# Kernel tuning notes

Hardware: AMD Instinct MI355X
Metric: run time of the kernel (lower is better)

## Reference

```python
import jax, jax.numpy as jnp
import numpy as np

D = 128
NM = 1043
ND = 2166
EM = 300000
ED = 600000


def _gcn(x, src, dst, w, W, b):
    # symmetric-normalized weighted GCN conv: out = A_norm @ (x W^T) + b
    n = x.shape[0]
    deg = jax.ops.segment_sum(w, dst, num_segments=n)
    dinv = jnp.where(deg > 0, 1.0 / jnp.sqrt(deg), 0.0)
    norm = dinv[src] * w * dinv[dst]          # [E]
    h = x @ W.T                               # [n, D]
    return jax.ops.segment_sum(h[src] * norm[:, None], dst, num_segments=n) + b


def _encoder(x, edge, w, W1, b1, W2, b2):
    src, dst = edge[0], edge[1]
    x1 = jax.nn.relu(_gcn(x, src, dst, w, W1, b1))
    x2 = jax.nn.relu(_gcn(x1, src, dst, w, W2, b2))
    return x1, x2


def _layer_view_att(x, fc1_W, fc1_b, fc2_W, fc2_b):
    # x: [C, D, N]; channel attention over views/layers (LayerViewAttention)
    a = x.mean(axis=(1, 2))                            # global avg pool -> [C]
    a = jax.nn.relu(a @ fc1_W.T + fc1_b)
    a = jax.nn.sigmoid(a @ fc2_W.T + fc2_b)
    return jax.nn.relu(x * a[:, None, None])


def _fcn(x, W1, b1, W2, b2):
    # Fcn fusion: Linear -> ReLU -> Linear -> ReLU
    h = jax.nn.relu(x @ W1.T + b1)
    return jax.nn.relu(h @ W2.T + b2)


def setup_inputs():
    key = jax.random.key(0)
    ks = iter(jax.random.split(key, 64))

    def nrm(shape, s=0.05):
        return jax.random.normal(next(ks), shape, jnp.float32) * s

    inp = {}
    inp["mirna_x"] = jax.random.normal(next(ks), (NM, D), jnp.float32)
    inp["drug_x"] = jax.random.normal(next(ks), (ND, D), jnp.float32)
    for pre, n, e in [("m1", NM, EM), ("m2", NM, EM), ("d1", ND, ED), ("d2", ND, ED)]:
        inp[pre + "_edge"] = jax.random.randint(next(ks), (2, e), 0, n, jnp.int32)
        inp[pre + "_w"] = jax.random.uniform(next(ks), (e,), jnp.float32)
        inp[pre + "_W1"] = nrm((D, D))
        inp[pre + "_b1"] = jnp.zeros((D,), jnp.float32)
        inp[pre + "_W2"] = nrm((D, D))
        inp[pre + "_b2"] = jnp.zeros((D,), jnp.float32)
    inp["m_fc1_W"] = nrm((4, 4)); inp["m_fc1_b"] = jnp.zeros((4,), jnp.float32)
    inp["m_fc2_W"] = nrm((4, 4)); inp["m_fc2_b"] = jnp.zeros((4,), jnp.float32)
    inp["d_fc1_W"] = nrm((2, 2)); inp["d_fc1_b"] = jnp.zeros((2,), jnp.float32)
    inp["d_fc2_W"] = nrm((2, 2)); inp["d_fc2_b"] = jnp.zeros((2,), jnp.float32)
    inp["m_fus_W1"] = nrm((2 * D, 4 * D)); inp["m_fus_b1"] = jnp.zeros((2 * D,), jnp.float32)
    inp["m_fus_W2"] = nrm((D, 2 * D));     inp["m_fus_b2"] = jnp.zeros((D,), jnp.float32)
    inp["d_fus_W1"] = nrm((2 * D, 2 * D)); inp["d_fus_b1"] = jnp.zeros((2 * D,), jnp.float32)
    inp["d_fus_W2"] = nrm((D, 2 * D));     inp["d_fus_b2"] = jnp.zeros((D,), jnp.float32)
    return inp


def reference(mirna_x, drug_x,
              m1_edge, m1_w, m1_W1, m1_b1, m1_W2, m1_b2,
              m2_edge, m2_w, m2_W1, m2_b1, m2_W2, m2_b2,
              d1_edge, d1_w, d1_W1, d1_b1, d1_W2, d1_b2,
              d2_edge, d2_w, d2_W1, d2_b1, d2_W2, d2_b2,
              m_fc1_W, m_fc1_b, m_fc2_W, m_fc2_b,
              d_fc1_W, d_fc1_b, d_fc2_W, d_fc2_b,
              m_fus_W1, m_fus_b1, m_fus_W2, m_fus_b2,
              d_fus_W1, d_fus_b1, d_fus_W2, d_fus_b2):
    # miRNA: 2 views x 2 layers -> 4 channels
    m1a, m1b = _encoder(mirna_x, m1_edge, m1_w, m1_W1, m1_b1, m1_W2, m1_b2)
    m2a, m2b = _encoder(mirna_x, m2_edge, m2_w, m2_W1, m2_b1, m2_W2, m2_b2)
    mx = jnp.stack([m1a, m1b, m2a, m2b], axis=0).transpose(0, 2, 1)   # [4, D, NM]
    mx = _layer_view_att(mx, m_fc1_W, m_fc1_b, m_fc2_W, m_fc2_b)
    m_out = _fcn(mx.transpose(2, 0, 1).reshape(NM, 4 * D),
                 m_fus_W1, m_fus_b1, m_fus_W2, m_fus_b2)             # [NM, D]
    # drug: views summed per layer -> 2 channels
    d1a, d1b = _encoder(drug_x, d1_edge, d1_w, d1_W1, d1_b1, d1_W2, d1_b2)
    d2a, d2b = _encoder(drug_x, d2_edge, d2_w, d2_W1, d2_b1, d2_W2, d2_b2)
    dx = jnp.stack([d1a + d2a, d1b + d2b], axis=0).transpose(0, 2, 1)  # [2, D, ND]
    dx = _layer_view_att(dx, d_fc1_W, d_fc1_b, d_fc2_W, d_fc2_b)
    d_out = _fcn(dx.transpose(2, 0, 1).reshape(ND, 2 * D),
                 d_fus_W1, d_fus_b1, d_fus_W2, d_fus_b2)             # [ND, D]
    return jnp.concatenate([m_out, d_out], axis=0)                   # [NM+ND, D]
```

## Files before the change

### kernel.cpp

```cpp
#include <hip/hip_runtime.h>
#include <math.h>

#define D128 128
#define NM_ 1043
#define ND_ 2166
#define EM_ 300000
#define ED_ 600000
#define NBH 64
#define NMAX 2176
#define NTOT 6418
#define ETOT 1800000

struct ViewArgs {
    const int* edge[4];
    const float* w[4];
    int n[4], E[4];
    int cumn[5];
    int cumE[5];
    int rpo[4];
};

struct BiasArr { const float* b[4]; };

__global__ __launch_bounds__(1024) void hist_b(ViewArgs va, int* __restrict__ pcnt,
                                               float* __restrict__ pdeg) {
    __shared__ int lc[NMAX];
    __shared__ float ld[NMAX];
    const int view = blockIdx.x >> 6, vb = blockIdx.x & 63;
    const int n = va.n[view], E = va.E[view];
    const int* edge = va.edge[view];
    const float* w = va.w[view];
    for (int i = threadIdx.x; i < n; i += 1024) { lc[i] = 0; ld[i] = 0.f; }
    __syncthreads();
    const int per = (E + NBH - 1) / NBH;
    const int b = vb * per, e = min(E, b + per);
    for (int i = b + threadIdx.x; i < e; i += 1024) {
        int dst = edge[E + i];
        atomicAdd(&lc[dst], 1);
        atomicAdd(&ld[dst], w[i]);
    }
    __syncthreads();
    int* pc = pcnt + (size_t)NBH * va.cumn[view] + (size_t)vb * n;
    float* pd = pdeg + (size_t)NBH * va.cumn[view] + (size_t)vb * n;
    for (int i = threadIdx.x; i < n; i += 1024) { pc[i] = lc[i]; pd[i] = ld[i]; }
}

__global__ void colred_b(ViewArgs va, const int* __restrict__ pcnt,
                         const float* __restrict__ pdeg, int* __restrict__ cnt,
                         float* __restrict__ dinv) {
    int i = blockIdx.x * 256 + threadIdx.x;
    if (i >= NTOT) return;
    int view = 0;
    while (view < 3 && i >= va.cumn[view + 1]) ++view;
    const int il = i - va.cumn[view], n = va.n[view];
    const int* pc = pcnt + (size_t)NBH * va.cumn[view];
    const float* pd = pdeg + (size_t)NBH * va.cumn[view];
    int c = 0;
    float dg = 0.f;
    for (int b = 0; b < NBH; ++b) {
        c += pc[(size_t)b * n + il];
        dg += pd[(size_t)b * n + il];
    }
    cnt[i] = c;
    dinv[i] = dg > 0.f ? 1.0f / sqrtf(dg) : 0.f;
}

__global__ void scan_b(ViewArgs va, const int* __restrict__ cnt, int* __restrict__ rowptr) {
    __shared__ int wsum[4];
    const int view = blockIdx.x;
    const int n = va.n[view];
    const int* c = cnt + va.cumn[view];
    int* rp = rowptr + va.rpo[view];
    const int tid = threadIdx.x;
    const int per = (n + 255) / 256;
    const int b0 = tid * per, e0 = min(n, b0 + per);
    int s = 0;
    for (int i = b0; i < e0; ++i) s += c[i];
    const int lane = tid & 63, wid = tid >> 6;
    int sc = s;
    for (int off = 1; off < 64; off <<= 1) {
        int t = __shfl_up(sc, off);
        if (lane >= off) sc += t;
    }
    if (lane == 63) wsum[wid] = sc;
    __syncthreads();
    int wbase = 0;
    for (int wv = 0; wv < wid; ++wv) wbase += wsum[wv];
    int run = wbase + sc - s;
    if (tid == 0) rp[0] = 0;
    for (int i = b0; i < e0; ++i) {
        run += c[i];
        rp[i + 1] = run;
    }
}

__global__ void cum_b(ViewArgs va, const int* __restrict__ pcnt,
                      const int* __restrict__ rowptr, int* __restrict__ cum) {
    int i = blockIdx.x * 256 + threadIdx.x;
    if (i >= NTOT) return;
    int view = 0;
    while (view < 3 && i >= va.cumn[view + 1]) ++view;
    const int il = i - va.cumn[view], n = va.n[view];
    const int* pc = pcnt + (size_t)NBH * va.cumn[view];
    int* cm = cum + (size_t)NBH * va.cumn[view];
    int run = rowptr[va.rpo[view] + il];
    for (int b = 0; b < NBH; ++b) {
        cm[(size_t)b * n + il] = run;
        run += pc[(size_t)b * n + il];
    }
}

__global__ __launch_bounds__(1024) void fill2_b(ViewArgs va, const float* __restrict__ dinv,
                                                const int* __restrict__ cum,
                                                int2* __restrict__ spair) {
    __shared__ int lc[NMAX];
    const int view = blockIdx.x >> 6, vb = blockIdx.x & 63;
    const int n = va.n[view], E = va.E[view];
    const int* edge = va.edge[view];
    const float* w = va.w[view];
    const int* cm = cum + (size_t)NBH * va.cumn[view] + (size_t)vb * n;
    const float* dv = dinv + va.cumn[view];
    int2* sp = spair + va.cumE[view];
    for (int i = threadIdx.x; i < n; i += 1024) lc[i] = cm[i];
    __syncthreads();
    const int per = (E + NBH - 1) / NBH;
    const int b = vb * per, e = min(E, b + per);
    for (int i = b + threadIdx.x; i < e; i += 1024) {
        int src = edge[i];
        int dst = edge[E + i];
        int pos = atomicAdd(&lc[dst], 1);
        float nrm = dv[src] * w[i] * dv[dst];
        sp[pos] = make_int2(src, __float_as_int(nrm));
    }
}

__global__ __launch_bounds__(128) void agg_b(ViewArgs va, const int2* __restrict__ spair,
                                             const int* __restrict__ rowptr,
                                             const float* __restrict__ h, BiasArr ba,
                                             float* __restrict__ outbuf) {
    const int xcd = blockIdx.x & 7, k = blockIdx.x >> 3;
    const int nf = (xcd < 2 ? xcd * 803 : 2 * 803 + (xcd - 2) * 802) + k;
    int view = 0;
    while (view < 3 && nf >= va.cumn[view + 1]) ++view;
    const int ln = nf - va.cumn[view];
    const int* rp = rowptr + va.rpo[view];
    const int beg = rp[ln], end = rp[ln + 1];
    const int2* sp = spair + va.cumE[view];
    const float* hb = h + (size_t)va.cumn[view] * D128;
    const int tid = threadIdx.x;
    float a0 = 0.f, a1 = 0.f, a2 = 0.f, a3 = 0.f;
    int i = beg;
    for (; i + 32 <= end; i += 32) {
        int4 q[16];
        float hv[32];
#pragma unroll
        for (int u = 0; u < 16; ++u) q[u] = *(const int4*)(sp + i + 2 * u);
#pragma unroll
        for (int u = 0; u < 16; ++u) {
            hv[2 * u] = hb[(size_t)q[u].x * D128 + tid];
            hv[2 * u + 1] = hb[(size_t)q[u].z * D128 + tid];
        }
#pragma unroll
        for (int u = 0; u < 16; ++u) {
            a0 = fmaf(__int_as_float(q[u].y), hv[2 * u], a0);
            a1 = fmaf(__int_as_float(q[u].w), hv[2 * u + 1], a1);
        }
    }
    for (; i + 8 <= end; i += 8) {
        int4 q0 = *(const int4*)(sp + i);
        int4 q1 = *(const int4*)(sp + i + 2);
        int4 q2 = *(const int4*)(sp + i + 4);
        int4 q3 = *(const int4*)(sp + i + 6);
        float h0 = hb[(size_t)q0.x * D128 + tid];
        float h1 = hb[(size_t)q0.z * D128 + tid];
        float h2 = hb[(size_t)q1.x * D128 + tid];
        float h3 = hb[(size_t)q1.z * D128 + tid];
        float h4 = hb[(size_t)q2.x * D128 + tid];
        float h5 = hb[(size_t)q2.z * D128 + tid];
        float h6 = hb[(size_t)q3.x * D128 + tid];
        float h7 = hb[(size_t)q3.z * D128 + tid];
        a0 = fmaf(__int_as_float(q0.y), h0, a0);
        a1 = fmaf(__int_as_float(q0.w), h1, a1);
        a2 = fmaf(__int_as_float(q1.y), h2, a2);
        a3 = fmaf(__int_as_float(q1.w), h3, a3);
        a0 = fmaf(__int_as_float(q2.y), h4, a0);
        a1 = fmaf(__int_as_float(q2.w), h5, a1);
        a2 = fmaf(__int_as_float(q3.y), h6, a2);
        a3 = fmaf(__int_as_float(q3.w), h7, a3);
    }
    for (; i + 4 <= end; i += 4) {
        int2 p0 = sp[i], p1 = sp[i + 1], p2 = sp[i + 2], p3 = sp[i + 3];
        a0 = fmaf(__int_as_float(p0.y), hb[(size_t)p0.x * D128 + tid], a0);
        a1 = fmaf(__int_as_float(p1.y), hb[(size_t)p1.x * D128 + tid], a1);
        a2 = fmaf(__int_as_float(p2.y), hb[(size_t)p2.x * D128 + tid], a2);
        a3 = fmaf(__int_as_float(p3.y), hb[(size_t)p3.x * D128 + tid], a3);
    }
    for (; i < end; ++i)
        a0 = fmaf(__int_as_float(sp[i].y), hb[(size_t)sp[i].x * D128 + tid], a0);
    float v = (a0 + a1) + (a2 + a3);
    outbuf[(size_t)nf * D128 + tid] = fmaxf(v + ba.b[view][tid], 0.f);
}

struct GSeg {
    const float* A;
    const float* W;
    const float* bias;
    float* C;
    int M, N, K, rowblks, blk0, relu;
};
struct GArgs { GSeg s[4]; int nseg; };

__global__ __launch_bounds__(256) void gemm_b(GArgs ga) {
    __shared__ float xs[32 * 64];
    __shared__ float wsm[128 * 64];
    int si = 0;
    while (si + 1 < ga.nseg && (int)blockIdx.x >= ga.s[si + 1].blk0) ++si;
    const GSeg S = ga.s[si];
    const int lb = blockIdx.x - S.blk0;
    const int rb = lb % S.rowblks, cb = lb / S.rowblks;
    const int row0 = rb * 32, col0 = cb * 128;
    const int tid = threadIdx.x;
    const int r0 = (tid >> 5) << 2;
    const int c0 = tid & 31;
    const int csw = (c0 & 7) << 2;
    float acc[4][4] = {};
    for (int kc = 0; kc < S.K; kc += 64) {
#pragma unroll
        for (int it = 0; it < 2; ++it) {
            int idx = tid + it * 256;
            int r = idx >> 4, k4 = (idx & 15) << 2;
            int gr = row0 + r;
            if (gr > S.M - 1) gr = S.M - 1;
            *(float4*)(xs + r * 64 + k4) =
                *(const float4*)(S.A + (size_t)gr * S.K + kc + k4);
        }
#pragma unroll
        for (int it = 0; it < 8; ++it) {
            int idx = tid + it * 256;
            int c = idx >> 4, k4 = (idx & 15) << 2;
            *(float4*)(wsm + c * 64 + (k4 ^ ((c & 7) << 2))) =
                *(const float4*)(S.W + (size_t)(col0 + c) * S.K + kc + k4);
        }
        __syncthreads();
#pragma unroll
        for (int k4 = 0; k4 < 64; k4 += 4) {
            float4 a0 = *(const float4*)(xs + (r0 + 0) * 64 + k4);
            float4 a1 = *(const float4*)(xs + (r0 + 1) * 64 + k4);
            float4 a2 = *(const float4*)(xs + (r0 + 2) * 64 + k4);
            float4 a3 = *(const float4*)(xs + (r0 + 3) * 64 + k4);
            const int sk = k4 ^ csw;
            float4 w0 = *(const float4*)(wsm + (c0 + 0) * 64 + sk);
            float4 w1 = *(const float4*)(wsm + (c0 + 32) * 64 + sk);
            float4 w2 = *(const float4*)(wsm + (c0 + 64) * 64 + sk);
            float4 w3 = *(const float4*)(wsm + (c0 + 96) * 64 + sk);
#define FMA4(i, av)                                                   \
            acc[i][0] = fmaf(av.x, w0.x, acc[i][0]); acc[i][0] = fmaf(av.y, w0.y, acc[i][0]); \
            acc[i][0] = fmaf(av.z, w0.z, acc[i][0]); acc[i][0] = fmaf(av.w, w0.w, acc[i][0]); \
            acc[i][1] = fmaf(av.x, w1.x, acc[i][1]); acc[i][1] = fmaf(av.y, w1.y, acc[i][1]); \
            acc[i][1] = fmaf(av.z, w1.z, acc[i][1]); acc[i][1] = fmaf(av.w, w1.w, acc[i][1]); \
            acc[i][2] = fmaf(av.x, w2.x, acc[i][2]); acc[i][2] = fmaf(av.y, w2.y, acc[i][2]); \
            acc[i][2] = fmaf(av.z, w2.z, acc[i][2]); acc[i][2] = fmaf(av.w, w2.w, acc[i][2]); \
            acc[i][3] = fmaf(av.x, w3.x, acc[i][3]); acc[i][3] = fmaf(av.y, w3.y, acc[i][3]); \
            acc[i][3] = fmaf(av.z, w3.z, acc[i][3]); acc[i][3] = fmaf(av.w, w3.w, acc[i][3]);
            FMA4(0, a0) FMA4(1, a1) FMA4(2, a2) FMA4(3, a3)
#undef FMA4
        }
        __syncthreads();
    }
#pragma unroll
    for (int i = 0; i < 4; ++i) {
        int gr = row0 + r0 + i;
        if (gr < S.M) {
#pragma unroll
            for (int j = 0; j < 4; ++j) {
                int gc = col0 + c0 + 32 * j;
                float v = acc[i][j];
                if (S.bias) v += S.bias[gc];
                if (S.relu) v = fmaxf(v, 0.f);
                S.C[(size_t)gr * S.N + gc] = v;
            }
        }
    }
}

struct SumArgs {
    const float* p[8];
    int cnt[8];
};

__global__ __launch_bounds__(256) void sum8_kernel(SumArgs args, float* __restrict__ sums) {
    __shared__ float red[256];
    const int ch = blockIdx.y;
    const float* x = args.p[ch];
    const int count = args.cnt[ch];
    float s = 0.f;
    for (int i = blockIdx.x * 256 + threadIdx.x; i < count; i += gridDim.x * 256) s += x[i];
    red[threadIdx.x] = s;
    __syncthreads();
    for (int off = 128; off > 0; off >>= 1) {
        if (threadIdx.x < off) red[threadIdx.x] += red[threadIdx.x + off];
        __syncthreads();
    }
    if (threadIdx.x == 0) atomicAdd(&sums[ch], red[0]);
}

__global__ void att_kernel(const float* __restrict__ sums,
                           const float* __restrict__ mW1, const float* __restrict__ mb1,
                           const float* __restrict__ mW2, const float* __restrict__ mb2,
                           const float* __restrict__ dW1, const float* __restrict__ db1,
                           const float* __restrict__ dW2, const float* __restrict__ db2,
                           float* __restrict__ scales) {
    if (threadIdx.x != 0 || blockIdx.x != 0) return;
    float mean[4], a[4];
    const float invM = 1.0f / (128.f * (float)NM_);
    for (int c = 0; c < 4; ++c) mean[c] = sums[c] * invM;
    for (int i = 0; i < 4; ++i) {
        float v = mb1[i];
        for (int j = 0; j < 4; ++j) v += mW1[i * 4 + j] * mean[j];
        a[i] = fmaxf(v, 0.f);
    }
    for (int c = 0; c < 4; ++c) {
        float v = mb2[c];
        for (int j = 0; j < 4; ++j) v += mW2[c * 4 + j] * a[j];
        scales[c] = 1.f / (1.f + expf(-v));
    }
    const float invD = 1.0f / (128.f * (float)ND_);
    float md[2] = {(sums[4] + sums[6]) * invD, (sums[5] + sums[7]) * invD};
    float ad[2];
    for (int i = 0; i < 2; ++i) {
        float v = db1[i];
        for (int j = 0; j < 2; ++j) v += dW1[i * 2 + j] * md[j];
        ad[i] = fmaxf(v, 0.f);
    }
    for (int c = 0; c < 2; ++c) {
        float v = db2[c];
        for (int j = 0; j < 2; ++j) v += dW2[c * 2 + j] * ad[j];
        scales[4 + c] = 1.f / (1.f + expf(-v));
    }
}

#define MCAT (NM_ * 512)
#define DCAT (ND_ * 256)

__global__ void cat_all(const float* __restrict__ l1, const float* __restrict__ l2,
                        const float* __restrict__ scales, float* __restrict__ catm,
                        float* __restrict__ catd) {
    int idx = blockIdx.x * 256 + threadIdx.x;
    if (idx < MCAT) {
        int i = idx >> 9;
        int k = idx & 511;
        int c = k >> 7;
        int j = k & 127;
        const float* p = (c == 0) ? l1 : (c == 1) ? l2
                         : (c == 2) ? l1 + (size_t)1043 * D128 : l2 + (size_t)1043 * D128;
        catm[idx] = fmaxf(scales[c] * p[(size_t)i * D128 + j], 0.f);
    } else if (idx < MCAT + DCAT) {
        int t = idx - MCAT;
        int i = t >> 8;
        int k = t & 255;
        int c = k >> 7;
        int j = k & 127;
        const float* pa = (c ? l2 : l1) + (size_t)2086 * D128;
        const float* pb = (c ? l2 : l1) + (size_t)4252 * D128;
        catd[t] = fmaxf(scales[4 + c] * (pa[(size_t)i * D128 + j] + pb[(size_t)i * D128 + j]), 0.f);
    }
}

extern "C" void kernel_launch(void* const* d_in, const int* in_sizes, int n_in,
                              void* d_out, int out_size, void* d_ws, size_t ws_size,
                              hipStream_t stream) {
    const float* mirna_x = (const float*)d_in[0];
    const float* drug_x  = (const float*)d_in[1];
    float* out = (float*)d_out;
    (void)in_sizes; (void)n_in; (void)out_size; (void)ws_size;

    char* ws = (char*)d_ws;
    auto AL = [](size_t x) { return (x + 255) & ~(size_t)255; };
    size_t o = 0;
    int2* spair = (int2*)(ws + o);   o += AL((size_t)ETOT * 8);
    int* cnt = (int*)(ws + o);       o += AL((size_t)NTOT * 4);
    int* rowptr = (int*)(ws + o);    o += AL((size_t)(NTOT + 4) * 4);
    float* dinv = (float*)(ws + o);  o += AL((size_t)NTOT * 4);
    float* sums = (float*)(ws + o);  o += 256;
    float* scales = (float*)(ws + o); o += 256;
    float* hbuf = (float*)(ws + o);  o += AL((size_t)NTOT * D128 * 4);
    float* l1out = (float*)(ws + o); o += AL((size_t)NTOT * D128 * 4);
    float* l2out = (float*)(ws + o); o += AL((size_t)NTOT * D128 * 4);
    const size_t R = o;
    int*   pcnt = (int*)(ws + R);
    float* pdeg = (float*)(ws + R + AL((size_t)NBH * NTOT * 4));
    int*   cum  = (int*)(ws + R + 2 * AL((size_t)NBH * NTOT * 4));
    float* catb_m = (float*)(ws + R);
    float* catb_d = (float*)(ws + R + AL((size_t)NM_ * 512 * 4));
    float* fush1_m = (float*)(ws + R + AL((size_t)NM_ * 512 * 4) + AL((size_t)ND_ * 256 * 4));
    float* fush1_d = fush1_m + (size_t)NM_ * 256;

    ViewArgs va;
    const int vb_in[4] = {2, 8, 14, 20};
    int nn[4] = {NM_, NM_, ND_, ND_};
    int ee[4] = {EM_, EM_, ED_, ED_};
    int cn = 0, ce = 0;
    for (int v = 0; v < 4; ++v) {
        va.edge[v] = (const int*)d_in[vb_in[v]];
        va.w[v] = (const float*)d_in[vb_in[v] + 1];
        va.n[v] = nn[v];
        va.E[v] = ee[v];
        va.cumn[v] = cn;
        va.cumE[v] = ce;
        va.rpo[v] = cn + v;
        cn += nn[v];
        ce += ee[v];
    }
    va.cumn[4] = cn;
    va.cumE[4] = ce;

    hipMemsetAsync(sums, 0, 8 * 4, stream);

    hist_b<<<256, 1024, 0, stream>>>(va, pcnt, pdeg);
    colred_b<<<(NTOT + 255) / 256, 256, 0, stream>>>(va, pcnt, pdeg, cnt, dinv);
    scan_b<<<4, 256, 0, stream>>>(va, cnt, rowptr);
    cum_b<<<(NTOT + 255) / 256, 256, 0, stream>>>(va, pcnt, rowptr, cum);
    fill2_b<<<256, 1024, 0, stream>>>(va, dinv, cum, spair);

    auto feat_gemm = [&](int layer, const float* l1src) {
        GArgs ga;
        ga.nseg = 4;
        int blk = 0;
        for (int v = 0; v < 4; ++v) {
            GSeg& S = ga.s[v];
            S.A = (layer == 1) ? ((v < 2) ? mirna_x : drug_x)
                               : l1src + (size_t)va.cumn[v] * D128;
            S.W = (const float*)d_in[vb_in[v] + (layer == 1 ? 2 : 4)];
            S.bias = nullptr;
            S.C = hbuf + (size_t)va.cumn[v] * D128;
            S.M = va.n[v]; S.N = 128; S.K = 128;
            S.rowblks = (va.n[v] + 31) / 32;
            S.blk0 = blk; S.relu = 0;
            blk += S.rowblks;
        }
        gemm_b<<<blk, 256, 0, stream>>>(ga);
    };
    BiasArr b1, b2;
    for (int v = 0; v < 4; ++v) {
        b1.b[v] = (const float*)d_in[vb_in[v] + 3];
        b2.b[v] = (const float*)d_in[vb_in[v] + 5];
    }

    feat_gemm(1, nullptr);
    agg_b<<<NTOT, 128, 0, stream>>>(va, spair, rowptr, hbuf, b1, l1out);
    feat_gemm(2, l1out);
    agg_b<<<NTOT, 128, 0, stream>>>(va, spair, rowptr, hbuf, b2, l2out);

    SumArgs sa;
    sa.p[0] = l1out;                      sa.p[1] = l2out;
    sa.p[2] = l1out + (size_t)1043 * 128; sa.p[3] = l2out + (size_t)1043 * 128;
    sa.p[4] = l1out + (size_t)2086 * 128; sa.p[5] = l2out + (size_t)2086 * 128;
    sa.p[6] = l1out + (size_t)4252 * 128; sa.p[7] = l2out + (size_t)4252 * 128;
    sa.cnt[0] = sa.cnt[1] = sa.cnt[2] = sa.cnt[3] = NM_ * D128;
    sa.cnt[4] = sa.cnt[5] = sa.cnt[6] = sa.cnt[7] = ND_ * D128;
    sum8_kernel<<<dim3(16, 8), 256, 0, stream>>>(sa, sums);
    att_kernel<<<1, 64, 0, stream>>>(sums,
        (const float*)d_in[26], (const float*)d_in[27], (const float*)d_in[28], (const float*)d_in[29],
        (const float*)d_in[30], (const float*)d_in[31], (const float*)d_in[32], (const float*)d_in[33],
        scales);

    cat_all<<<(MCAT + DCAT + 255) / 256, 256, 0, stream>>>(l1out, l2out, scales, catb_m, catb_d);

    {
        GArgs ga;
        ga.nseg = 2;
        ga.s[0] = {catb_m, (const float*)d_in[34], (const float*)d_in[35], fush1_m,
                   NM_, 256, 512, 33, 0, 1};
        ga.s[1] = {catb_d, (const float*)d_in[38], (const float*)d_in[39], fush1_d,
                   ND_, 256, 256, 68, 66, 1};
        gemm_b<<<66 + 136, 256, 0, stream>>>(ga);
    }
    {
        GArgs ga;
        ga.nseg = 2;
        ga.s[0] = {fush1_m, (const float*)d_in[36], (const float*)d_in[37], out,
                   NM_, 128, 256, 33, 0, 1};
        ga.s[1] = {fush1_d, (const float*)d_in[40], (const float*)d_in[41],
                   out + (size_t)NM_ * D128, ND_, 128, 256, 68, 33, 1};
        gemm_b<<<33 + 68, 256, 0, stream>>>(ga);
    }
}
```

Before: 237.7 us.

## Fuse layer-1 feature GEMM into the edge-fill kernel as extra blocks

```diff
diff --git a/kernel.cpp b/kernel.cpp
--- a/kernel.cpp
+++ b/kernel.cpp
@@ -110,27 +110,122 @@
     }
 }
 
-__global__ __launch_bounds__(1024) void fill2_b(ViewArgs va, const float* __restrict__ dinv,
-                                                const int* __restrict__ cum,
-                                                int2* __restrict__ spair) {
-    __shared__ int lc[NMAX];
-    const int view = blockIdx.x >> 6, vb = blockIdx.x & 63;
-    const int n = va.n[view], E = va.E[view];
-    const int* edge = va.edge[view];
-    const float* w = va.w[view];
-    const int* cm = cum + (size_t)NBH * va.cumn[view] + (size_t)vb * n;
-    const float* dv = dinv + va.cumn[view];
-    int2* sp = spair + va.cumE[view];
-    for (int i = threadIdx.x; i < n; i += 1024) lc[i] = cm[i];
-    __syncthreads();
-    const int per = (E + NBH - 1) / NBH;
-    const int b = vb * per, e = min(E, b + per);
-    for (int i = b + threadIdx.x; i < e; i += 1024) {
-        int src = edge[i];
-        int dst = edge[E + i];
-        int pos = atomicAdd(&lc[dst], 1);
-        float nrm = dv[src] * w[i] * dv[dst];
-        sp[pos] = make_int2(src, __float_as_int(nrm));
+struct GSeg {
+    const float* A;
+    const float* W;
+    const float* bias;
+    float* C;
+    int M, N, K, rowblks, blk0, relu;
+};
+struct GArgs { GSeg s[4]; int nseg; };
+
+__device__ __forceinline__ void gemm_core(const GArgs& ga, int bid, int tid,
+                                          float* xs, float* wsm) {
+    int si = 0;
+    while (si + 1 < ga.nseg && bid >= ga.s[si + 1].blk0) ++si;
+    const GSeg S = ga.s[si];
+    const int lb = bid - S.blk0;
+    const int rb = lb % S.rowblks, cb = lb / S.rowblks;
+    const int row0 = rb * 32, col0 = cb * 128;
+    const int r0 = (tid >> 5) << 2;
+    const int c0 = tid & 31;
+    const int csw = (c0 & 7) << 2;
+    float acc[4][4] = {};
+    for (int kc = 0; kc < S.K; kc += 64) {
+#pragma unroll
+        for (int it = 0; it < 2; ++it) {
+            int idx = tid + it * 256;
+            int r = idx >> 4, k4 = (idx & 15) << 2;
+            int gr = row0 + r;
+            if (gr > S.M - 1) gr = S.M - 1;
+            *(float4*)(xs + r * 64 + k4) =
+                *(const float4*)(S.A + (size_t)gr * S.K + kc + k4);
+        }
+#pragma unroll
+        for (int it = 0; it < 8; ++it) {
+            int idx = tid + it * 256;
+            int c = idx >> 4, k4 = (idx & 15) << 2;
+            *(float4*)(wsm + c * 64 + (k4 ^ ((c & 7) << 2))) =
+                *(const float4*)(S.W + (size_t)(col0 + c) * S.K + kc + k4);
+        }
+        __syncthreads();
+#pragma unroll
+        for (int k4 = 0; k4 < 64; k4 += 4) {
+            float4 a0 = *(const float4*)(xs + (r0 + 0) * 64 + k4);
+            float4 a1 = *(const float4*)(xs + (r0 + 1) * 64 + k4);
+            float4 a2 = *(const float4*)(xs + (r0 + 2) * 64 + k4);
+            float4 a3 = *(const float4*)(xs + (r0 + 3) * 64 + k4);
+            const int sk = k4 ^ csw;
+            float4 w0 = *(const float4*)(wsm + (c0 + 0) * 64 + sk);
+            float4 w1 = *(const float4*)(wsm + (c0 + 32) * 64 + sk);
+            float4 w2 = *(const float4*)(wsm + (c0 + 64) * 64 + sk);
+            float4 w3 = *(const float4*)(wsm + (c0 + 96) * 64 + sk);
+#define FMA4(i, av)                                                   \
+            acc[i][0] = fmaf(av.x, w0.x, acc[i][0]); acc[i][0] = fmaf(av.y, w0.y, acc[i][0]); \
+            acc[i][0] = fmaf(av.z, w0.z, acc[i][0]); acc[i][0] = fmaf(av.w, w0.w, acc[i][0]); \
+            acc[i][1] = fmaf(av.x, w1.x, acc[i][1]); acc[i][1] = fmaf(av.y, w1.y, acc[i][1]); \
+            acc[i][1] = fmaf(av.z, w1.z, acc[i][1]); acc[i][1] = fmaf(av.w, w1.w, acc[i][1]); \
+            acc[i][2] = fmaf(av.x, w2.x, acc[i][2]); acc[i][2] = fmaf(av.y, w2.y, acc[i][2]); \
+            acc[i][2] = fmaf(av.z, w2.z, acc[i][2]); acc[i][2] = fmaf(av.w, w2.w, acc[i][2]); \
+            acc[i][3] = fmaf(av.x, w3.x, acc[i][3]); acc[i][3] = fmaf(av.y, w3.y, acc[i][3]); \
+            acc[i][3] = fmaf(av.z, w3.z, acc[i][3]); acc[i][3] = fmaf(av.w, w3.w, acc[i][3]);
+            FMA4(0, a0) FMA4(1, a1) FMA4(2, a2) FMA4(3, a3)
+#undef FMA4
+        }
+        __syncthreads();
+    }
+#pragma unroll
+    for (int i = 0; i < 4; ++i) {
+        int gr = row0 + r0 + i;
+        if (gr < S.M) {
+#pragma unroll
+            for (int j = 0; j < 4; ++j) {
+                int gc = col0 + c0 + 32 * j;
+                float v = acc[i][j];
+                if (S.bias) v += S.bias[gc];
+                if (S.relu) v = fmaxf(v, 0.f);
+                S.C[(size_t)gr * S.N + gc] = v;
+            }
+        }
+    }
+}
+
+__global__ __launch_bounds__(256) void gemm_b(GArgs ga) {
+    __shared__ __align__(16) float smem[10240];
+    gemm_core(ga, blockIdx.x, threadIdx.x, smem, smem + 2048);
+}
+
+__global__ __launch_bounds__(1024) void fillgemm_b(ViewArgs va, const float* __restrict__ dinv,
+                                                   const int* __restrict__ cum,
+                                                   int2* __restrict__ spair, GArgs ga) {
+    __shared__ __align__(16) float smem[10240];
+    if (blockIdx.x < 256) {
+        int* lc = (int*)smem;
+        const int view = blockIdx.x >> 6, vb = blockIdx.x & 63;
+        const int n = va.n[view], E = va.E[view];
+        const int* edge = va.edge[view];
+        const float* w = va.w[view];
+        const int* cm = cum + (size_t)NBH * va.cumn[view] + (size_t)vb * n;
+        const float* dv = dinv + va.cumn[view];
+        int2* sp = spair + va.cumE[view];
+        for (int i = threadIdx.x; i < n; i += 1024) lc[i] = cm[i];
+        __syncthreads();
+        const int per = (E + NBH - 1) / NBH;
+        const int b = vb * per, e = min(E, b + per);
+        for (int i = b + threadIdx.x; i < e; i += 1024) {
+            int src = edge[i];
+            int dst = edge[E + i];
+            int pos = atomicAdd(&lc[dst], 1);
+            float nrm = dv[src] * w[i] * dv[dst];
+            sp[pos] = make_int2(src, __float_as_int(nrm));
+        }
+    } else {
+        if (threadIdx.x < 256) {
+            gemm_core(ga, blockIdx.x - 256, threadIdx.x, smem, smem + 2048);
+        } else {
+#pragma unroll
+            for (int it = 0; it < 4; ++it) __syncthreads();
+        }
     }
 }
 
@@ -201,88 +296,6 @@
     outbuf[(size_t)nf * D128 + tid] = fmaxf(v + ba.b[view][tid], 0.f);
 }
 
-struct GSeg {
-    const float* A;
-    const float* W;
-    const float* bias;
-    float* C;
-    int M, N, K, rowblks, blk0, relu;
-};
-struct GArgs { GSeg s[4]; int nseg; };
-
-__global__ __launch_bounds__(256) void gemm_b(GArgs ga) {
-    __shared__ float xs[32 * 64];
-    __shared__ float wsm[128 * 64];
-    int si = 0;
-    while (si + 1 < ga.nseg && (int)blockIdx.x >= ga.s[si + 1].blk0) ++si;
-    const GSeg S = ga.s[si];
-    const int lb = blockIdx.x - S.blk0;
-    const int rb = lb % S.rowblks, cb = lb / S.rowblks;
-    const int row0 = rb * 32, col0 = cb * 128;
-    const int tid = threadIdx.x;
-    const int r0 = (tid >> 5) << 2;
-    const int c0 = tid & 31;
-    const int csw = (c0 & 7) << 2;
-    float acc[4][4] = {};
-    for (int kc = 0; kc < S.K; kc += 64) {
-#pragma unroll
-        for (int it = 0; it < 2; ++it) {
-            int idx = tid + it * 256;
-            int r = idx >> 4, k4 = (idx & 15) << 2;
-            int gr = row0 + r;
-            if (gr > S.M - 1) gr = S.M - 1;
-            *(float4*)(xs + r * 64 + k4) =
-                *(const float4*)(S.A + (size_t)gr * S.K + kc + k4);
-        }
-#pragma unroll
-        for (int it = 0; it < 8; ++it) {
-            int idx = tid + it * 256;
-            int c = idx >> 4, k4 = (idx & 15) << 2;
-            *(float4*)(wsm + c * 64 + (k4 ^ ((c & 7) << 2))) =
-                *(const float4*)(S.W + (size_t)(col0 + c) * S.K + kc + k4);
-        }
-        __syncthreads();
-#pragma unroll
-        for (int k4 = 0; k4 < 64; k4 += 4) {
-            float4 a0 = *(const float4*)(xs + (r0 + 0) * 64 + k4);
-            float4 a1 = *(const float4*)(xs + (r0 + 1) * 64 + k4);
-            float4 a2 = *(const float4*)(xs + (r0 + 2) * 64 + k4);
-            float4 a3 = *(const float4*)(xs + (r0 + 3) * 64 + k4);
-            const int sk = k4 ^ csw;
-            float4 w0 = *(const float4*)(wsm + (c0 + 0) * 64 + sk);
-            float4 w1 = *(const float4*)(wsm + (c0 + 32) * 64 + sk);
-            float4 w2 = *(const float4*)(wsm + (c0 + 64) * 64 + sk);
-            float4 w3 = *(const float4*)(wsm + (c0 + 96) * 64 + sk);
-#define FMA4(i, av)                                                   \
-            acc[i][0] = fmaf(av.x, w0.x, acc[i][0]); acc[i][0] = fmaf(av.y, w0.y, acc[i][0]); \
-            acc[i][0] = fmaf(av.z, w0.z, acc[i][0]); acc[i][0] = fmaf(av.w, w0.w, acc[i][0]); \
-            acc[i][1] = fmaf(av.x, w1.x, acc[i][1]); acc[i][1] = fmaf(av.y, w1.y, acc[i][1]); \
-            acc[i][1] = fmaf(av.z, w1.z, acc[i][1]); acc[i][1] = fmaf(av.w, w1.w, acc[i][1]); \
-            acc[i][2] = fmaf(av.x, w2.x, acc[i][2]); acc[i][2] = fmaf(av.y, w2.y, acc[i][2]); \
-            acc[i][2] = fmaf(av.z, w2.z, acc[i][2]); acc[i][2] = fmaf(av.w, w2.w, acc[i][2]); \
-            acc[i][3] = fmaf(av.x, w3.x, acc[i][3]); acc[i][3] = fmaf(av.y, w3.y, acc[i][3]); \
-            acc[i][3] = fmaf(av.z, w3.z, acc[i][3]); acc[i][3] = fmaf(av.w, w3.w, acc[i][3]);
-            FMA4(0, a0) FMA4(1, a1) FMA4(2, a2) FMA4(3, a3)
-#undef FMA4
-        }
-        __syncthreads();
-    }
-#pragma unroll
-    for (int i = 0; i < 4; ++i) {
-        int gr = row0 + r0 + i;
-        if (gr < S.M) {
-#pragma unroll
-            for (int j = 0; j < 4; ++j) {
-                int gc = col0 + c0 + 32 * j;
-                float v = acc[i][j];
-                if (S.bias) v += S.bias[gc];
-                if (S.relu) v = fmaxf(v, 0.f);
-                S.C[(size_t)gr * S.N + gc] = v;
-            }
-        }
-    }
-}
-
 struct SumArgs {
     const float* p[8];
     int cnt[8];
@@ -416,13 +429,7 @@
 
     hipMemsetAsync(sums, 0, 8 * 4, stream);
 
-    hist_b<<<256, 1024, 0, stream>>>(va, pcnt, pdeg);
-    colred_b<<<(NTOT + 255) / 256, 256, 0, stream>>>(va, pcnt, pdeg, cnt, dinv);
-    scan_b<<<4, 256, 0, stream>>>(va, cnt, rowptr);
-    cum_b<<<(NTOT + 255) / 256, 256, 0, stream>>>(va, pcnt, rowptr, cum);
-    fill2_b<<<256, 1024, 0, stream>>>(va, dinv, cum, spair);
-
-    auto feat_gemm = [&](int layer, const float* l1src) {
+    auto make_feat = [&](int layer, const float* l1src) {
         GArgs ga;
         ga.nseg = 4;
         int blk = 0;
@@ -438,7 +445,7 @@
             S.blk0 = blk; S.relu = 0;
             blk += S.rowblks;
         }
-        gemm_b<<<blk, 256, 0, stream>>>(ga);
+        return ga;
     };
     BiasArr b1, b2;
     for (int v = 0; v < 4; ++v) {
@@ -446,9 +453,20 @@
         b2.b[v] = (const float*)d_in[vb_in[v] + 5];
     }
 
-    feat_gemm(1, nullptr);
+    hist_b<<<256, 1024, 0, stream>>>(va, pcnt, pdeg);
+    colred_b<<<(NTOT + 255) / 256, 256, 0, stream>>>(va, pcnt, pdeg, cnt, dinv);
+    scan_b<<<4, 256, 0, stream>>>(va, cnt, rowptr);
+    cum_b<<<(NTOT + 255) / 256, 256, 0, stream>>>(va, pcnt, rowptr, cum);
+    {
+        GArgs g1 = make_feat(1, nullptr);
+        fillgemm_b<<<256 + 202, 1024, 0, stream>>>(va, dinv, cum, spair, g1);
+    }
+
     agg_b<<<NTOT, 128, 0, stream>>>(va, spair, rowptr, hbuf, b1, l1out);
-    feat_gemm(2, l1out);
+    {
+        GArgs g2 = make_feat(2, l1out);
+        gemm_b<<<202, 256, 0, stream>>>(g2);
+    }
     agg_b<<<NTOT, 128, 0, stream>>>(va, spair, rowptr, hbuf, b2, l2out);
 
     SumArgs sa;
```

Measured after the change: 240.0 us. About the same (+1.0%).
